# Kernel optimization log

Measured on AMD Instinct MI355X. Metric: run time of the kernel, lower is better.

Reference implementation:

```python
import jax, jax.numpy as jnp
import numpy as np

N = 100000   # nodes
E = 3200000  # edges
D = 128      # in_channels
H = 128      # hidden_channels
G = 512      # graphs in batch
C = 10       # classes (hardcoded in module)


def setup_inputs() -> dict:
    key = jax.random.key(0)
    ks = jax.random.split(key, 9)
    x = jax.random.normal(ks[0], (N, D), jnp.float32)
    edge_index = jax.random.randint(ks[1], (2, E), 0, N, jnp.int32)
    batch = jnp.sort(jax.random.randint(ks[2], (N,), 0, G, jnp.int32))
    def lin(k, fi, fo):
        s = 1.0 / np.sqrt(fi)
        kw, kb = jax.random.split(k)
        return (jax.random.uniform(kw, (fi, fo), jnp.float32, -s, s),
                jax.random.uniform(kb, (fo,), jnp.float32, -s, s))
    W1, b1 = lin(ks[3], D, H)
    W2, b2 = lin(ks[4], H, H)
    Wout, bout = lin(ks[5], H, C)
    return {"x": x, "W1": W1, "b1": b1, "W2": W2, "b2": b2,
            "Wout": Wout, "bout": bout,
            "edge_index": edge_index, "batch": batch}


def _gcn_layer(x, W, b, row, col):
    # PyG GCNConv: linear transform, add self-loops, sym-normalize, scatter-add at col.
    x = x @ W
    loop = jnp.arange(N, dtype=row.dtype)
    r = jnp.concatenate([row, loop])
    c = jnp.concatenate([col, loop])
    deg = jax.ops.segment_sum(jnp.ones(r.shape, x.dtype), c, num_segments=N)
    dinv = jnp.where(deg > 0, jax.lax.rsqrt(deg), 0.0)
    norm = (dinv[r] * dinv[c])[:, None]          # [E+N, 1]
    out = jax.ops.segment_sum(x[r] * norm, c, num_segments=N)  # gather-scale-scatter
    return out + b


def reference(x, W1, b1, W2, b2, Wout, bout, edge_index, batch):
    row, col = edge_index[0], edge_index[1]
    h = jax.nn.relu(_gcn_layer(x, W1, b1, row, col))
    # dropout p=0.5 skipped (eval mode, training=False)
    h = jax.nn.relu(_gcn_layer(h, W2, b2, row, col))
    cnt = jax.ops.segment_sum(jnp.ones((N,), h.dtype), batch, num_segments=G)
    pooled = jax.ops.segment_sum(h, batch, num_segments=G) / jnp.maximum(cnt, 1.0)[:, None]
    logits = pooled @ Wout + bout                # [G, 10]
    return jax.nn.log_softmax(logits, axis=1)
```

## Files before the change

### kernel.cpp

```cpp
#include <hip/hip_runtime.h>
#include <hip/hip_bf16.h>

constexpr int N_ = 100000;
constexpr int E_ = 3200000;
constexpr int HD = 128;
constexpr int G_ = 512;
constexpr int C_ = 10;

constexpr int NB  = 782;
constexpr int CAP = 6144;
constexpr int ITEMS = E_ + N_;

typedef __bf16  bf16x8 __attribute__((ext_vector_type(8)));
typedef float   f32x4  __attribute__((ext_vector_type(4)));

__device__ __forceinline__ float b2f_lo(unsigned u) { return __uint_as_float(u << 16); }
__device__ __forceinline__ float b2f_hi(unsigned u) { return __uint_as_float(u & 0xFFFF0000u); }
__device__ __forceinline__ unsigned short f2b(float f) {
    unsigned u = __float_as_uint(f);
    u += 0x7FFFu + ((u >> 16) & 1u);
    return (unsigned short)(u >> 16);
}

__global__ __launch_bounds__(256) void k_scatter(const int* __restrict__ ei,
                                                 int* __restrict__ cursor,
                                                 unsigned int* __restrict__ staging) {
    __shared__ int lhist[NB];
    __shared__ int lbase[NB];
    const int t = threadIdx.x;
    const int per = (ITEMS + gridDim.x - 1) / gridDim.x;
    const int start = blockIdx.x * per;
    const int end = min(start + per, ITEMS);
    for (int b = t; b < NB; b += 256) lhist[b] = 0;
    __syncthreads();
    for (int i = start + t; i < end; i += 256) {
        int c = (i < E_) ? ei[E_ + i] : (i - E_);
        atomicAdd(&lhist[c >> 7], 1);
    }
    __syncthreads();
    for (int b = t; b < NB; b += 256) {
        int cnt = lhist[b];
        lbase[b] = (cnt > 0) ? atomicAdd(&cursor[b], cnt) : 0;
        lhist[b] = 0;
    }
    __syncthreads();
    for (int i = start + t; i < end; i += 256) {
        int r, c;
        if (i < E_) { r = ei[i]; c = ei[E_ + i]; }
        else        { r = c = i - E_; }
        int b = c >> 7;
        int pos = lbase[b] + atomicAdd(&lhist[b], 1);
        if (pos < CAP)
            staging[(size_t)b * CAP + pos] =
                ((unsigned)(c & 127) << 17) | (unsigned)r;
    }
}

__global__ __launch_bounds__(1024) void k_scanb(const int* __restrict__ cursor,
                                                int* __restrict__ bstart,
                                                int* __restrict__ off) {
    __shared__ int s[1024];
    const int t = threadIdx.x;
    s[t] = (t < NB) ? cursor[t] : 0;
    __syncthreads();
    for (int d = 1; d < 1024; d <<= 1) {
        int v = (t >= d) ? s[t - d] : 0;
        __syncthreads();
        s[t] += v;
        __syncthreads();
    }
    if (t < NB) bstart[t] = s[t] - cursor[t];
    if (t == 0) { bstart[NB] = ITEMS; off[N_] = ITEMS; }
}

__global__ __launch_bounds__(256) void k_finalize(const unsigned int* __restrict__ staging,
                                                  const int* __restrict__ cursor,
                                                  const int* __restrict__ bstart,
                                                  int* __restrict__ off,
                                                  float* __restrict__ dinv,
                                                  int* __restrict__ src) {
    __shared__ int ldeg[128];
    __shared__ int loff[128];
    __shared__ int lcur[128];
    const int b = blockIdx.x;
    const int t = threadIdx.x;
    const int cnt = min(cursor[b], CAP);
    const int base = bstart[b];
    if (t < 128) ldeg[t] = 0;
    __syncthreads();
    for (int i = t; i < cnt; i += 256)
        atomicAdd(&ldeg[staging[(size_t)b * CAP + i] >> 17], 1);
    __syncthreads();
    if (t == 0) {
        int run = 0;
        for (int l = 0; l < 128; ++l) { loff[l] = run; run += ldeg[l]; }
    }
    __syncthreads();
    if (t < 128) {
        int node = b * 128 + t;
        if (node < N_) {
            off[node] = base + loff[t];
            dinv[node] = rsqrtf((float)ldeg[t]);
        }
        lcur[t] = loff[t];
    }
    __syncthreads();
    for (int i = t; i < cnt; i += 256) {
        unsigned item = staging[(size_t)b * CAP + i];
        int cl = item >> 17;
        int r = (int)(item & 0x1FFFFu);
        int pos = atomicAdd(&lcur[cl], 1);
        src[base + pos] = r;
    }
}

__global__ __launch_bounds__(256) void k_prepW(const float* __restrict__ W,
                                               unsigned short* __restrict__ wf) {
    const int s = blockIdx.x * 256 + threadIdx.x;
    if (s >= 2048) return;
    const int ks   = s >> 9;
    const int rem  = s & 511;
    const int nt   = rem >> 6;
    const int lane = rem & 63;
    const int kb = ks * 32 + (lane >> 4) * 8;
    const int n  = nt * 16 + (lane & 15);
    unsigned short tmp[8];
#pragma unroll
    for (int i = 0; i < 8; ++i) tmp[i] = f2b(W[(size_t)(kb + i) * HD + n]);
    uint4 o;
    o.x = (unsigned)tmp[0] | ((unsigned)tmp[1] << 16);
    o.y = (unsigned)tmp[2] | ((unsigned)tmp[3] << 16);
    o.z = (unsigned)tmp[4] | ((unsigned)tmp[5] << 16);
    o.w = (unsigned)tmp[6] | ((unsigned)tmp[7] << 16);
    *reinterpret_cast<uint4*>(wf + (size_t)s * 8) = o;
}

template <bool XBF16>
__global__ __launch_bounds__(256) void k_gemm_mfma(const void* __restrict__ Xv,
                                                   const unsigned short* __restrict__ wf,
                                                   const float* __restrict__ dinv,
                                                   unsigned short* __restrict__ Y,
                                                   int nrows) {
    const int t = threadIdx.x;
    const int wid = t >> 6;
    const int lane = t & 63;
    const int rowbase = blockIdx.x * 64 + wid * 16;
    const int arow = rowbase + (lane & 15);
    const int aoff = (lane >> 4) * 8;

    f32x4 acc[8];
#pragma unroll
    for (int nt = 0; nt < 8; ++nt) acc[nt] = f32x4{0.f, 0.f, 0.f, 0.f};

#pragma unroll
    for (int ks = 0; ks < 4; ++ks) {
        bf16x8 af;
        if constexpr (XBF16) {
            uint4 raw = make_uint4(0, 0, 0, 0);
            if (arow < nrows) {
                const unsigned short* X = (const unsigned short*)Xv;
                raw = *reinterpret_cast<const uint4*>(X + (size_t)arow * HD + ks * 32 + aoff);
            }
            af = __builtin_bit_cast(bf16x8, raw);
        } else {
            float4 v0 = make_float4(0.f, 0.f, 0.f, 0.f);
            float4 v1 = make_float4(0.f, 0.f, 0.f, 0.f);
            if (arow < nrows) {
                const float* X = (const float*)Xv;
                const float* p = X + (size_t)arow * HD + ks * 32 + aoff;
                v0 = *reinterpret_cast<const float4*>(p);
                v1 = *reinterpret_cast<const float4*>(p + 4);
            }
            af[0] = (__bf16)v0.x; af[1] = (__bf16)v0.y;
            af[2] = (__bf16)v0.z; af[3] = (__bf16)v0.w;
            af[4] = (__bf16)v1.x; af[5] = (__bf16)v1.y;
            af[6] = (__bf16)v1.z; af[7] = (__bf16)v1.w;
        }
#pragma unroll
        for (int nt = 0; nt < 8; ++nt) {
            uint4 braw = *reinterpret_cast<const uint4*>(
                wf + ((size_t)((ks * 8 + nt) * 64 + lane)) * 8);
            bf16x8 bf = __builtin_bit_cast(bf16x8, braw);
            acc[nt] = __builtin_amdgcn_mfma_f32_16x16x32_bf16(af, bf, acc[nt], 0, 0, 0);
        }
    }

    const int cbase = lane & 15;
    const int rgrp  = (lane >> 4) * 4;
#pragma unroll
    for (int reg = 0; reg < 4; ++reg) {
        const int orow = rowbase + rgrp + reg;
        if (orow < nrows) {
            const float s = dinv[orow];
#pragma unroll
            for (int nt = 0; nt < 8; ++nt)
                Y[(size_t)orow * HD + nt * 16 + cbase] = f2b(acc[nt][reg] * s);
        }
    }
}

__global__ __launch_bounds__(64) void k_agg(const unsigned short* __restrict__ xws,
                                            const int* __restrict__ off,
                                            const int* __restrict__ src,
                                            const float* __restrict__ dinv,
                                            const float* __restrict__ bias,
                                            unsigned short* __restrict__ out) {
    const int n = blockIdx.x;
    const int t = threadIdx.x;
    const int half = t >> 5;
    const int q = t & 31;
    __shared__ int sh[128];
    const int s0 = off[n];
    const int m = off[n + 1] - s0;
    float4 a0 = make_float4(0.f, 0.f, 0.f, 0.f);
    float4 a1 = make_float4(0.f, 0.f, 0.f, 0.f);
    for (int basei = 0; basei < m; basei += 128) {
        const int chunk = min(128, m - basei);
        if (t < chunk) sh[t] = src[s0 + basei + t];
        if (t + 64 < chunk) sh[t + 64] = src[s0 + basei + t + 64];
        __syncthreads();
        const int fp = chunk >> 1;
        int k = 0;
        for (; k + 8 <= fp; k += 8) {
            uint2 v[8];
#pragma unroll
            for (int u = 0; u < 8; ++u) {
                int r = sh[2 * (k + u) + half];
                v[u] = *reinterpret_cast<const uint2*>(xws + (size_t)r * HD + q * 4);
            }
#pragma unroll
            for (int u = 0; u < 8; ++u) {
                float4& a = (u & 1) ? a1 : a0;
                a.x += b2f_lo(v[u].x); a.y += b2f_hi(v[u].x);
                a.z += b2f_lo(v[u].y); a.w += b2f_hi(v[u].y);
            }
        }
        for (; k < fp; ++k) {
            int r = sh[2 * k + half];
            uint2 vv = *reinterpret_cast<const uint2*>(xws + (size_t)r * HD + q * 4);
            a0.x += b2f_lo(vv.x); a0.y += b2f_hi(vv.x);
            a0.z += b2f_lo(vv.y); a0.w += b2f_hi(vv.y);
        }
        if ((chunk & 1) && half == 0) {
            int r = sh[chunk - 1];
            uint2 vv = *reinterpret_cast<const uint2*>(xws + (size_t)r * HD + q * 4);
            a0.x += b2f_lo(vv.x); a0.y += b2f_hi(vv.x);
            a0.z += b2f_lo(vv.y); a0.w += b2f_hi(vv.y);
        }
        __syncthreads();
    }
    float4 acc;
    acc.x = a0.x + a1.x; acc.y = a0.y + a1.y;
    acc.z = a0.z + a1.z; acc.w = a0.w + a1.w;
    acc.x += __shfl_xor(acc.x, 32, 64);
    acc.y += __shfl_xor(acc.y, 32, 64);
    acc.z += __shfl_xor(acc.z, 32, 64);
    acc.w += __shfl_xor(acc.w, 32, 64);
    if (half == 0) {
        const float dn = dinv[n];
        float4 bb = reinterpret_cast<const float4*>(bias)[q];
        float r0 = fmaxf(acc.x * dn + bb.x, 0.f);
        float r1 = fmaxf(acc.y * dn + bb.y, 0.f);
        float r2 = fmaxf(acc.z * dn + bb.z, 0.f);
        float r3 = fmaxf(acc.w * dn + bb.w, 0.f);
        uint2 o;
        o.x = (unsigned)f2b(r0) | ((unsigned)f2b(r1) << 16);
        o.y = (unsigned)f2b(r2) | ((unsigned)f2b(r3) << 16);
        *reinterpret_cast<uint2*>(out + (size_t)n * HD + q * 4) = o;
    }
}

__global__ __launch_bounds__(64) void k_pool(const unsigned short* __restrict__ h,
                                             const int* __restrict__ batch,
                                             float* __restrict__ pooled) {
    const int g = blockIdx.x;
    const int t = threadIdx.x;
    const int half = t >> 5;
    const int q = t & 31;
    auto lb = [&](int key) {
        int lo = 0, hi = N_;
        while (lo < hi) {
            int mid = (lo + hi) >> 1;
            if (batch[mid] < key) lo = mid + 1; else hi = mid;
        }
        return lo;
    };
    const int lo = lb(g), hi = lb(g + 1);
    const int m = hi - lo;
    float4 a0 = make_float4(0.f, 0.f, 0.f, 0.f);
    float4 a1 = make_float4(0.f, 0.f, 0.f, 0.f);
    const int fp = m >> 1;
    int k = 0;
    for (; k + 4 <= fp; k += 4) {
        uint2 v[4];
#pragma unroll
        for (int u = 0; u < 4; ++u) {
            int rr = lo + 2 * (k + u) + half;
            v[u] = *reinterpret_cast<const uint2*>(h + (size_t)rr * HD + q * 4);
        }
#pragma unroll
        for (int u = 0; u < 4; ++u) {
            float4& a = (u & 1) ? a1 : a0;
            a.x += b2f_lo(v[u].x); a.y += b2f_hi(v[u].x);
            a.z += b2f_lo(v[u].y); a.w += b2f_hi(v[u].y);
        }
    }
    for (; k < fp; ++k) {
        int rr = lo + 2 * k + half;
        uint2 vv = *reinterpret_cast<const uint2*>(h + (size_t)rr * HD + q * 4);
        a0.x += b2f_lo(vv.x); a0.y += b2f_hi(vv.x);
        a0.z += b2f_lo(vv.y); a0.w += b2f_hi(vv.y);
    }
    if ((m & 1) && half == 0) {
        int rr = lo + m - 1;
        uint2 vv = *reinterpret_cast<const uint2*>(h + (size_t)rr * HD + q * 4);
        a0.x += b2f_lo(vv.x); a0.y += b2f_hi(vv.x);
        a0.z += b2f_lo(vv.y); a0.w += b2f_hi(vv.y);
    }
    float4 acc;
    acc.x = a0.x + a1.x; acc.y = a0.y + a1.y;
    acc.z = a0.z + a1.z; acc.w = a0.w + a1.w;
    acc.x += __shfl_xor(acc.x, 32, 64);
    acc.y += __shfl_xor(acc.y, 32, 64);
    acc.z += __shfl_xor(acc.z, 32, 64);
    acc.w += __shfl_xor(acc.w, 32, 64);
    if (half == 0) {
        const float inv = 1.0f / fmaxf((float)m, 1.0f);
        *reinterpret_cast<float4*>(pooled + (size_t)g * HD + q * 4) =
            make_float4(acc.x * inv, acc.y * inv, acc.z * inv, acc.w * inv);
    }
}

__global__ __launch_bounds__(64) void k_head(const float* __restrict__ pooled,
                                             const float* __restrict__ Wout,
                                             const float* __restrict__ bout,
                                             float* __restrict__ out) {
    const int g = blockIdx.x;
    const int t = threadIdx.x;
    __shared__ float sp[HD];
    __shared__ float sl[C_];
    sp[t] = pooled[(size_t)g * HD + t];
    sp[t + 64] = pooled[(size_t)g * HD + t + 64];
    __syncthreads();
    if (t < C_) {
        float d = bout[t];
        for (int k = 0; k < HD; ++k) d += sp[k] * Wout[k * C_ + t];
        sl[t] = d;
    }
    __syncthreads();
    if (t == 0) {
        float mx = sl[0];
        for (int c = 1; c < C_; ++c) mx = fmaxf(mx, sl[c]);
        float se = 0.f;
        for (int c = 0; c < C_; ++c) se += expf(sl[c] - mx);
        float lse = logf(se);
        for (int c = 0; c < C_; ++c) out[(size_t)g * C_ + c] = sl[c] - mx - lse;
    }
}


extern "C" void kernel_launch(void* const* d_in, const int* in_sizes, int n_in,
                              void* d_out, int out_size, void* d_ws, size_t ws_size,
                              hipStream_t stream) {
    const float* x    = (const float*)d_in[0];
    const float* W1   = (const float*)d_in[1];
    const float* b1   = (const float*)d_in[2];
    const float* W2   = (const float*)d_in[3];
    const float* b2   = (const float*)d_in[4];
    const float* Wout = (const float*)d_in[5];
    const float* bout = (const float*)d_in[6];
    const int*   ei   = (const int*)d_in[7];
    const int*   batch= (const int*)d_in[8];
    float* out = (float*)d_out;

    size_t o = 0;
    auto carve = [&](size_t bytes) {
        void* p = (char*)d_ws + o;
        o += (bytes + 15) & ~size_t(15);
        return p;
    };
    int*   cursor = (int*)carve(NB * 4);
    int*   bstart = (int*)carve((NB + 1) * 4);
    int*   off    = (int*)carve((N_ + 1) * 4);
    float* dinv   = (float*)carve(N_ * 4);
    int*   src    = (int*)carve((size_t)ITEMS * 4);
    unsigned short* wf1 = (unsigned short*)carve(2048 * 16);
    unsigned short* wf2 = (unsigned short*)carve(2048 * 16);
    unsigned short* bufA = (unsigned short*)carve((size_t)N_ * HD * 2);
    unsigned short* bufB = (unsigned short*)carve((size_t)N_ * HD * 2);
    float* pooled = (float*)carve((size_t)G_ * HD * 4);
    unsigned int* staging = (unsigned int*)bufA;

    hipMemsetAsync(cursor, 0, NB * sizeof(int), stream);
    k_prepW   <<<8, 256, 0, stream>>>(W1, wf1);
    k_prepW   <<<8, 256, 0, stream>>>(W2, wf2);
    k_scatter <<<512, 256, 0, stream>>>(ei, cursor, staging);
    k_scanb   <<<1, 1024, 0, stream>>>(cursor, bstart, off);
    k_finalize<<<NB, 256, 0, stream>>>(staging, cursor, bstart, off, dinv, src);

    const int gblk = (N_ + 63) / 64;
    k_gemm_mfma<false><<<gblk, 256, 0, stream>>>(x, wf1, dinv, bufA, N_);
    k_agg <<<N_, 64, 0, stream>>>(bufA, off, src, dinv, b1, bufB);
    k_gemm_mfma<true><<<gblk, 256, 0, stream>>>(bufB, wf2, dinv, bufA, N_);
    k_agg <<<N_, 64, 0, stream>>>(bufA, off, src, dinv, b2, bufB);
    k_pool<<<G_, 64, 0, stream>>>(bufB, batch, pooled);
    k_head<<<G_, 64, 0, stream>>>(pooled, Wout, bout, out);
}
```

Baseline: 566.3 us.

## Split neighbor aggregation into two feature-half passes for cache locality

The gather-aggregate kernel now runs twice per layer, each pass covering 64 of the 128 feature columns, with 4-byte loads per lane and a deeper 16-way unroll. The aim is to halve the working set of the gathered feature matrix in each pass (about 12.8 MB instead of 25.6 MB) so random neighbor rows hit L2/LLC more often. In exchange, the edge index list and offsets are read twice, launch count doubles, and each load is narrower, so more load instructions are issued per byte.

Result: slower. 683.7 us (+20.7%).

```diff
diff --git a/kernel.cpp b/kernel.cpp
--- a/kernel.cpp
+++ b/kernel.cpp
@@ -199,12 +199,13 @@
     }
 }
 
-__global__ __launch_bounds__(64) void k_agg(const unsigned short* __restrict__ xws,
-                                            const int* __restrict__ off,
-                                            const int* __restrict__ src,
-                                            const float* __restrict__ dinv,
-                                            const float* __restrict__ bias,
-                                            unsigned short* __restrict__ out) {
+__global__ __launch_bounds__(64) void k_agg_p(const unsigned short* __restrict__ xws,
+                                              const int* __restrict__ off,
+                                              const int* __restrict__ src,
+                                              const float* __restrict__ dinv,
+                                              const float* __restrict__ bias,
+                                              unsigned short* __restrict__ out,
+                                              int fo) {
     const int n = blockIdx.x;
     const int t = threadIdx.x;
     const int half = t >> 5;
@@ -212,8 +213,9 @@
     __shared__ int sh[128];
     const int s0 = off[n];
     const int m = off[n + 1] - s0;
-    float4 a0 = make_float4(0.f, 0.f, 0.f, 0.f);
-    float4 a1 = make_float4(0.f, 0.f, 0.f, 0.f);
+    const int foq = fo + q * 2;
+    float2 a0 = make_float2(0.f, 0.f);
+    float2 a1 = make_float2(0.f, 0.f);
     for (int basei = 0; basei < m; basei += 128) {
         const int chunk = min(128, m - basei);
         if (t < chunk) sh[t] = src[s0 + basei + t];
@@ -221,52 +223,41 @@
         __syncthreads();
         const int fp = chunk >> 1;
         int k = 0;
-        for (; k + 8 <= fp; k += 8) {
-            uint2 v[8];
-#pragma unroll
-            for (int u = 0; u < 8; ++u) {
+        for (; k + 16 <= fp; k += 16) {
+            unsigned v[16];
+#pragma unroll
+            for (int u = 0; u < 16; ++u) {
                 int r = sh[2 * (k + u) + half];
-                v[u] = *reinterpret_cast<const uint2*>(xws + (size_t)r * HD + q * 4);
+                v[u] = *reinterpret_cast<const unsigned*>(xws + (size_t)r * HD + foq);
             }
 #pragma unroll
-            for (int u = 0; u < 8; ++u) {
-                float4& a = (u & 1) ? a1 : a0;
-                a.x += b2f_lo(v[u].x); a.y += b2f_hi(v[u].x);
-                a.z += b2f_lo(v[u].y); a.w += b2f_hi(v[u].y);
+            for (int u = 0; u < 16; ++u) {
+                float2& a = (u & 1) ? a1 : a0;
+                a.x += b2f_lo(v[u]); a.y += b2f_hi(v[u]);
             }
         }
         for (; k < fp; ++k) {
             int r = sh[2 * k + half];
-            uint2 vv = *reinterpret_cast<const uint2*>(xws + (size_t)r * HD + q * 4);
-            a0.x += b2f_lo(vv.x); a0.y += b2f_hi(vv.x);
-            a0.z += b2f_lo(vv.y); a0.w += b2f_hi(vv.y);
+            unsigned vv = *reinterpret_cast<const unsigned*>(xws + (size_t)r * HD + foq);
+            a0.x += b2f_lo(vv); a0.y += b2f_hi(vv);
         }
         if ((chunk & 1) && half == 0) {
             int r = sh[chunk - 1];
-            uint2 vv = *reinterpret_cast<const uint2*>(xws + (size_t)r * HD + q * 4);
-            a0.x += b2f_lo(vv.x); a0.y += b2f_hi(vv.x);
-            a0.z += b2f_lo(vv.y); a0.w += b2f_hi(vv.y);
+            unsigned vv = *reinterpret_cast<const unsigned*>(xws + (size_t)r * HD + foq);
+            a0.x += b2f_lo(vv); a0.y += b2f_hi(vv);
         }
         __syncthreads();
     }
-    float4 acc;
-    acc.x = a0.x + a1.x; acc.y = a0.y + a1.y;
-    acc.z = a0.z + a1.z; acc.w = a0.w + a1.w;
+    float2 acc = make_float2(a0.x + a1.x, a0.y + a1.y);
     acc.x += __shfl_xor(acc.x, 32, 64);
     acc.y += __shfl_xor(acc.y, 32, 64);
-    acc.z += __shfl_xor(acc.z, 32, 64);
-    acc.w += __shfl_xor(acc.w, 32, 64);
     if (half == 0) {
         const float dn = dinv[n];
-        float4 bb = reinterpret_cast<const float4*>(bias)[q];
+        float2 bb = *reinterpret_cast<const float2*>(bias + foq);
         float r0 = fmaxf(acc.x * dn + bb.x, 0.f);
         float r1 = fmaxf(acc.y * dn + bb.y, 0.f);
-        float r2 = fmaxf(acc.z * dn + bb.z, 0.f);
-        float r3 = fmaxf(acc.w * dn + bb.w, 0.f);
-        uint2 o;
-        o.x = (unsigned)f2b(r0) | ((unsigned)f2b(r1) << 16);
-        o.y = (unsigned)f2b(r2) | ((unsigned)f2b(r3) << 16);
-        *reinterpret_cast<uint2*>(out + (size_t)n * HD + q * 4) = o;
+        unsigned o = (unsigned)f2b(r0) | ((unsigned)f2b(r1) << 16);
+        *reinterpret_cast<unsigned*>(out + (size_t)n * HD + foq) = o;
     }
 }
 
@@ -400,9 +391,11 @@
 
     const int gblk = (N_ + 63) / 64;
     k_gemm_mfma<false><<<gblk, 256, 0, stream>>>(x, wf1, dinv, bufA, N_);
-    k_agg <<<N_, 64, 0, stream>>>(bufA, off, src, dinv, b1, bufB);
+    k_agg_p<<<N_, 64, 0, stream>>>(bufA, off, src, dinv, b1, bufB, 0);
+    k_agg_p<<<N_, 64, 0, stream>>>(bufA, off, src, dinv, b1, bufB, 64);
     k_gemm_mfma<true><<<gblk, 256, 0, stream>>>(bufB, wf2, dinv, bufA, N_);
-    k_agg <<<N_, 64, 0, stream>>>(bufA, off, src, dinv, b2, bufB);
+    k_agg_p<<<N_, 64, 0, stream>>>(bufA, off, src, dinv, b2, bufB, 0);
+    k_agg_p<<<N_, 64, 0, stream>>>(bufA, off, src, dinv, b2, bufB, 64);
     k_pool<<<G_, 64, 0, stream>>>(bufB, batch, pooled);
     k_head<<<G_, 64, 0, stream>>>(pooled, Wout, bout, out);
 }
```
